# Optimization experiments

Measured on AMD Instinct MI355X. Metric: run time of the kernel, lower is better.

The kernel has to match this reference:

```python
import jax, jax.numpy as jnp
import numpy as np

G = 16          # graphs per side
NPG = 512       # nodes per graph
NSIDE = G * NPG # 8192 nodes per side
N = 2 * NSIDE   # 16384 nodes in combined batched graph
EPG = 4096      # edges per graph
E = 2 * G * EPG # 131072 edges
IN = 64; HID = 64; NH = 8; NC = 3
ALPHA = 0.2; EPS = 1e-5


def setup_inputs() -> dict:
    key = jax.random.key(0)
    ks = jax.random.split(key, 20)
    s = 0.05
    off = jnp.repeat(jnp.arange(2 * G, dtype=jnp.int32) * NPG, EPG)
    return {
        'nbd1': jax.random.normal(ks[0], (NSIDE, IN), jnp.float32),
        'nbd2': jax.random.normal(ks[1], (NSIDE, IN), jnp.float32),
        'ebd': jax.random.normal(ks[2], (E, IN), jnp.float32),
        'src': jax.random.randint(ks[3], (E,), 0, NPG, jnp.int32) + off,
        'dst': jax.random.randint(ks[4], (E,), 0, NPG, jnp.int32) + off,
        'node_gid': jnp.repeat(jnp.arange(2 * G, dtype=jnp.int32), NPG),
        'projW': jax.random.normal(ks[5], (4 * IN, HID), jnp.float32) * s,
        'W1': jax.random.normal(ks[6], (IN, NH * HID), jnp.float32) * s,
        'al1': jax.random.normal(ks[7], (NH, HID), jnp.float32) * s,
        'ar1': jax.random.normal(ks[8], (NH, HID), jnp.float32) * s,
        'ae1': jax.random.normal(ks[9], (NH, HID), jnp.float32) * s,
        'W2': jax.random.normal(ks[10], (NH * HID, NH * HID), jnp.float32) * s,
        'al2': jax.random.normal(ks[11], (NH, HID), jnp.float32) * s,
        'ar2': jax.random.normal(ks[12], (NH, HID), jnp.float32) * s,
        'ae2': jax.random.normal(ks[13], (NH, HID), jnp.float32) * s,
        'bn1_g': jnp.ones((2 * NH * HID,), jnp.float32),
        'bn1_b': jnp.zeros((2 * NH * HID,), jnp.float32),
        'fc1_W': jax.random.normal(ks[14], (2 * NH * HID, HID), jnp.float32) * s,
        'fc1_b': jnp.zeros((HID,), jnp.float32),
        'bn2_g': jnp.ones((HID,), jnp.float32),
        'bn2_b': jnp.zeros((HID,), jnp.float32),
        'fc2_W': jax.random.normal(ks[15], (HID, NC), jnp.float32) * s,
        'fc2_b': jnp.zeros((NC,), jnp.float32),
    }


def _segment_softmax(s, seg, n):
    # s: [E, H]; softmax over edges sharing the same destination node
    m = jax.ops.segment_max(s, seg, num_segments=n)
    ex = jnp.exp(s - m[seg])
    z = jax.ops.segment_sum(ex, seg, num_segments=n)
    return ex / jnp.maximum(z[seg], 1e-9)


def _gat_layer(hn, he, src, dst, n, W, al, ar, ae):
    nh, d = al.shape
    ft = (hn @ W).reshape(n, nh, d)            # [N,H,D]
    eft = (he @ W).reshape(-1, nh, d)          # [E,H,D]
    a1 = jnp.einsum('nhd,hd->nh', ft, al)
    a2 = jnp.einsum('nhd,hd->nh', ft, ar)
    a3 = jnp.einsum('ehd,hd->eh', eft, ae)
    a = a1[src] + a3 + a2[dst]                 # [E,H]
    a = jnp.where(a > 0, a, ALPHA * a)         # LeakyReLU(0.2)
    alpha = _segment_softmax(a, dst, n)[:, :, None]  # [E,H,1]
    f_cat = eft * alpha + ft[src] * alpha      # weighted edge + weighted src feat
    nft = jax.ops.segment_sum(f_cat, dst, num_segments=n)
    ret1 = jax.nn.elu(nft.reshape(n, nh * d))
    ret2 = jax.nn.elu(f_cat.reshape(f_cat.shape[0], nh * d))
    return ret1, ret2


def _bn(x, g, b):
    mu = jnp.mean(x, axis=0)
    v = jnp.var(x, axis=0)
    return (x - mu) * jax.lax.rsqrt(v + EPS) * g + b


def _forward(nbd1, nbd2, ebd, src, dst, node_gid, projW,
             W1, al1, ar1, ae1, W2, al2, ar2, ae2,
             bn1_g, bn1_b, fc1_W, fc1_b, bn2_g, bn2_b, fc2_W, fc2_b):
    # Node alignment (cross-graph soft attention, 2-D tensors as in source)
    att = nbd1 @ nbd2.T                                   # [N1,N2]
    x1a = jax.nn.softmax(att, axis=-1) @ nbd2
    x2a = jax.nn.softmax(att.T, axis=-1) @ nbd1
    q1 = jnp.concatenate([nbd1, x1a, nbd1 - x1a, nbd1 * x1a], axis=-1)
    q2 = jnp.concatenate([nbd2, x2a, nbd2 - x2a, nbd2 * x2a], axis=-1)
    h1 = jax.nn.relu(q1 @ projW)
    h2 = jax.nn.relu(q2 @ projW)
    h_n = jnp.concatenate([h1, h2], axis=0)               # [N,HID]
    h_e = ebd
    h_n, h_e = _gat_layer(h_n, h_e, src, dst, N, W1, al1, ar1, ae1)
    h_n, h_e = _gat_layer(h_n, h_e, src, dst, N, W2, al2, ar2, ae2)
    # dgl.mean_nodes
    cnt = jax.ops.segment_sum(jnp.ones((N,), h_n.dtype), node_gid, num_segments=2 * G)
    hg = jax.ops.segment_sum(h_n, node_gid, num_segments=2 * G) / cnt[:, None]
    x = jnp.concatenate([hg[:G], hg[G:2 * G]], axis=1)    # [G, 2*NH*HID]
    x = _bn(x, bn1_g, bn1_b)
    x = jax.nn.relu(x @ fc1_W + fc1_b)
    x = _bn(x, bn2_g, bn2_b)
    return x @ fc2_W + fc2_b                              # [G, NC]


def reference(nbd1, nbd2, ebd, src, dst, node_gid, projW,
              W1, al1, ar1, ae1, W2, al2, ar2, ae2,
              bn1_g, bn1_b, fc1_W, fc1_b, bn2_g, bn2_b, fc2_W, fc2_b):
    return _forward(nbd1, nbd2, ebd, src, dst, node_gid, projW,
                    W1, al1, ar1, ae1, W2, al2, ar2, ae2,
                    bn1_g, bn1_b, fc1_W, fc1_b, bn2_g, bn2_b, fc2_W, fc2_b)
```

## Files before the change

### kernel.cpp

```cpp
#include <hip/hip_runtime.h>


#define NSd 8192
#define NNd 16384
#define NEd 131072
#define KSPLIT 8

typedef unsigned short u16;
typedef unsigned int   u32;
typedef short bf16x8 __attribute__((ext_vector_type(8)));
typedef float f32x4  __attribute__((ext_vector_type(4)));
typedef float f32x16 __attribute__((ext_vector_type(16)));

__device__ __forceinline__ float bf2f(u16 u){ return __uint_as_float(((u32)u) << 16); }
__device__ __forceinline__ u16 f2bf(float f){
  u32 u = __float_as_uint(f);
  u += 0x7fffu + ((u >> 16) & 1u);
  return (u16)(u >> 16);
}
__device__ __forceinline__ u32 pkbf(float a, float b){
  u32 r;
  asm("v_cvt_pk_bf16_f32 %0, %1, %2" : "=v"(r) : "v"(a), "v"(b));
  return r;
}
__device__ __forceinline__ void pl32swap(u32& a, u32& b){
  auto r = __builtin_amdgcn_permlane32_swap(a, b, false, false);
  a = r[0]; b = r[1];
}
__device__ __forceinline__ float eluf(float x){ return x > 0.f ? x : expm1f(x); }
__device__ __forceinline__ float leaky(float x){ return x > 0.f ? x : 0.2f * x; }
__device__ __forceinline__ float ldin(const void* p, size_t i, int fl){
  return fl ? bf2f(((const u16*)p)[i]) : ((const float*)p)[i];
}
__device__ __forceinline__ void lse_merge(float& m, float& z, float om, float oz){
  float M = fmaxf(m, om);
  z = z * __expf(m - M) + oz * __expf(om - M);
  m = M;
}

static constexpr size_t OFF_WF   = 0;
static constexpr size_t OFF_CB   = 1529600;
static constexpr size_t OFF_U    = 1584896;
static constexpr size_t OFF_W1B  = 18362112;
static constexpr size_t OFF_W2B  = 18427648;
static constexpr size_t OFF_WE2B = 18951936;
static constexpr size_t OFF_WE1B = 18968320;
static constexpr size_t OFF_AL1  = 35139328;
static constexpr size_t OFF_SA   = 39333632;
static constexpr size_t OFF_HNA  = 43527936;
static constexpr size_t OFF_AN2  = 60305152;
static constexpr size_t OFF_DEG  = 77082368;
static constexpr size_t OFF_RP   = 77147904;
static constexpr size_t OFF_FILL = 77213696;
static constexpr size_t OFF_CIDX = 77279232;
static constexpr size_t OFF_RBIG = 77803520;
static constexpr size_t OFF_T    = 111357952;
static constexpr size_t OFF_XCAT = 144912384;
static constexpr size_t OFF_FLAG = 144977920;
static constexpr size_t WS_NEED  = 144978176;

static constexpr size_t T_X1A = 0;
static constexpr size_t T_X2A = 2097152;
static constexpr size_t T_HN0 = 4194304;
static constexpr size_t T_PZ  = 4194304;
static constexpr size_t T_AN1 = 8388608;
static constexpr size_t T_S   = 9437184;
static constexpr size_t T_Y   = 0;
static constexpr size_t T_Y1G = 0;
static constexpr size_t R_G2  = 16777216;

static constexpr int WO_PROJ = 0,      WO_W1 = 16384;
static constexpr int WO_AL1 = 49152,   WO_AR1 = 49664,  WO_AE1 = 50176;
static constexpr int WO_W2  = 50688;
static constexpr int WO_AL2 = 312832,  WO_AR2 = 313344, WO_AE2 = 313856;
static constexpr int WO_B1G = 314368,  WO_B1B = 315392;
static constexpr int WO_F1W = 316416,  WO_F1B = 381952;
static constexpr int WO_B2G = 382016,  WO_B2B = 382080;
static constexpr int WO_F2W = 382144,  WO_F2B = 382336;
static constexpr int WO_END = 382339;

static constexpr int CB_WC1 = 0;
static constexpr int CB_WE1 = 1024;
static constexpr int CB_WC2 = 1536;
static constexpr int CB_WE2 = 9728;
static constexpr int CB_END = 13824;

__global__ __launch_bounds__(256) void detect_k(const u16* __restrict__ p, int* __restrict__ flag){
  __shared__ int bad;
  if (threadIdx.x == 0) bad = 0;
  __syncthreads();
  int b = 0;
  for (int i = threadIdx.x; i < 1024; i += 256){
    float f = bf2f(p[i]);
    if (!(fabsf(f) <= 100.f)) b++;
  }
  atomicAdd(&bad, b);
  __syncthreads();
  if (threadIdx.x == 0) *flag = (bad == 0) ? 1 : 0;
}

struct P17 { const void* p[17]; };

__global__ __launch_bounds__(256) void convw_k(P17 ps, float* __restrict__ wf, const int* __restrict__ flagp){
  const int i = blockIdx.x * 256 + threadIdx.x;
  if (i >= WO_END) return;
  const int fl = *flagp;
  const int ends[17] = {16384,49152,49664,50176,50688,312832,313344,313856,314368,
                        315392,316416,381952,382016,382080,382144,382336,382339};
  int seg = 0;
  while (i >= ends[seg]) seg++;
  const int start = seg ? ends[seg-1] : 0;
  wf[i] = ldin(ps.p[seg], i - start, fl);
}

__global__ __launch_bounds__(256) void wprep_k(const float* __restrict__ wf, u16* __restrict__ w1t,
                                               u16* __restrict__ w2t, float* __restrict__ cb,
                                               u16* __restrict__ we2b, u16* __restrict__ we1b){
  const int i = blockIdx.x * 256 + threadIdx.x;
  if (i < 32768){
    const int c = i >> 6, k = i & 63;
    w1t[i] = f2bf(wf[WO_W1 + k * 512 + c]);
    return;
  }
  if (i < 294912){
    const int j = i - 32768;
    const int c = j >> 9, k = j & 511;
    w2t[j] = f2bf(wf[WO_W2 + k * 512 + c]);
    return;
  }
  const int j = i - 294912;
  if (j >= CB_END + 4096 + 512) return;
  if (j >= CB_END + 4096){ we1b[512 + (j - CB_END - 4096)] = 0; return; }
  if (j >= CB_END){ we2b[4096 + (j - CB_END)] = 0; return; }
  float acc = 0.f;
  if (j < 1024){
    const int o = j >> 6, d = j & 63, h = o & 7;
    const float* a = wf + ((o >> 3) ? WO_AR1 : WO_AL1) + h * 64;
    for (int dp = 0; dp < 64; dp++) acc += wf[WO_W1 + d * 512 + h * 64 + dp] * a[dp];
    cb[CB_WC1 + j] = acc;
  } else if (j < 1536){
    const int jj = j - 1024, h = jj >> 6, d = jj & 63;
    for (int dp = 0; dp < 64; dp++) acc += wf[WO_W1 + d * 512 + h * 64 + dp] * wf[WO_AE1 + h * 64 + dp];
    cb[CB_WE1 + jj] = acc;
    we1b[jj] = f2bf(acc);
  } else if (j < 9728){
    const int jj = j - 1536, o = jj >> 9, c = jj & 511, h = o & 7;
    for (int dp = 0; dp < 64; dp++){
      const float av = (o >> 3) ? wf[WO_AR2 + h * 64 + dp]
                                : (wf[WO_AL2 + h * 64 + dp] - wf[WO_AE2 + h * 64 + dp]);
      acc += wf[WO_W2 + c * 512 + h * 64 + dp] * av;
    }
    cb[CB_WC2 + jj] = acc;
  } else {
    const int jj = j - 9728, h = jj >> 9, c = jj & 511;
    for (int dp = 0; dp < 64; dp++) acc += wf[WO_W2 + c * 512 + h * 64 + dp] * wf[WO_AE2 + h * 64 + dp];
    cb[CB_WE2 + jj] = acc;
    we2b[jj] = f2bf(acc);
  }
}

__global__ __launch_bounds__(256) void flash_mfma_k(const void* __restrict__ Qp, const void* __restrict__ Kp,
                                                    const int* __restrict__ flagp, float* __restrict__ pacc,
                                                    float* __restrict__ pz){
  const int fl = *flagp;
  __shared__ __align__(16) u16 Ks[2][32][64];
  __shared__ __align__(16) u16 Kt[2][64][40];
  const int t = threadIdx.x;
  const int w = t >> 6, l = t & 63;
  const int hi = l >> 5, ql = l & 31;
  const int q0 = blockIdx.x * 128;
  const int kbeg = blockIdx.y * 1024;
  const int sr = t & 31, scg = t >> 5;
  const int kp = t & 15, dq = t >> 4;

  bf16x8 bq[4];
  {
    const int qrow = q0 + w * 32 + ql;
    if (fl){
      const u16* qp = (const u16*)Qp + (size_t)qrow * 64 + hi * 8;
      #pragma unroll
      for (int s = 0; s < 4; s++) bq[s] = *(const bf16x8*)(qp + s * 16);
    } else {
      const float* qp = (const float*)Qp + (size_t)qrow * 64 + hi * 8;
      #pragma unroll
      for (int s = 0; s < 4; s++){
        union { u32 w_[4]; bf16x8 v; } u;
        #pragma unroll
        for (int i = 0; i < 4; i++) u.w_[i] = pkbf(qp[s*16 + 2*i], qp[s*16 + 2*i + 1]);
        bq[s] = u.v;
      }
    }
  }

  f32x16 accO0, accO1;
  #pragma unroll
  for (int i = 0; i < 16; i++){ accO0[i] = 0.f; accO1[i] = 0.f; }
  float lsum = 0.f;

  {
    const int kr = kbeg;
    if (fl){
      const u16* kb = (const u16*)Kp + (size_t)kr * 64;
      const uint4 s0 = *(const uint4*)(kb + (size_t)sr * 64 + scg * 8);
      const uint2 a0 = *(const uint2*)(kb + (size_t)(2*kp) * 64 + dq * 4);
      const uint2 b0 = *(const uint2*)(kb + (size_t)(2*kp + 1) * 64 + dq * 4);
      *(uint4*)((char*)&Ks[0][sr][0] + ((scg * 16) ^ ((sr & 7) << 4))) = s0;
      const u16* pa = (const u16*)&a0; const u16* pb = (const u16*)&b0;
      #pragma unroll
      for (int i = 0; i < 4; i++)
        *(u32*)&Kt[0][4*dq + i][2*kp] = (u32)pa[i] | ((u32)pb[i] << 16);
    } else {
      const float* kf = (const float*)Kp + (size_t)kr * 64;
      const float4 f0 = *(const float4*)(kf + (size_t)sr * 64 + scg * 8);
      const float4 f1 = *(const float4*)(kf + (size_t)sr * 64 + scg * 8 + 4);
      const float4 fa = *(const float4*)(kf + (size_t)(2*kp) * 64 + dq * 4);
      const float4 fb = *(const float4*)(kf + (size_t)(2*kp + 1) * 64 + dq * 4);
      union { u32 w_[4]; uint4 q; } uu;
      uu.w_[0] = pkbf(f0.x, f0.y); uu.w_[1] = pkbf(f0.z, f0.w);
      uu.w_[2] = pkbf(f1.x, f1.y); uu.w_[3] = pkbf(f1.z, f1.w);
      *(uint4*)((char*)&Ks[0][sr][0] + ((scg * 16) ^ ((sr & 7) << 4))) = uu.q;
      const float* faf = &fa.x; const float* fbf = &fb.x;
      #pragma unroll
      for (int i = 0; i < 4; i++)
        *(u32*)&Kt[0][4*dq + i][2*kp] = pkbf(faf[i], fbf[i]);
    }
  }

  for (int it = 0; it < 32; it++){
    const int cur = it & 1;
    __syncthreads();

    uint4 nKs; uint2 nKa, nKb;
    float4 nKsf0, nKsf1, nKaf, nKbf;
    const bool nx = (it + 1 < 32);
    if (nx){
      const int kr = kbeg + (it + 1) * 32;
      if (fl){
        const u16* kb = (const u16*)Kp + (size_t)kr * 64;
        nKs = *(const uint4*)(kb + (size_t)sr * 64 + scg * 8);
        nKa = *(const uint2*)(kb + (size_t)(2*kp) * 64 + dq * 4);
        nKb = *(const uint2*)(kb + (size_t)(2*kp + 1) * 64 + dq * 4);
      } else {
        const float* kf = (const float*)Kp + (size_t)kr * 64;
        nKsf0 = *(const float4*)(kf + (size_t)sr * 64 + scg * 8);
        nKsf1 = *(const float4*)(kf + (size_t)sr * 64 + scg * 8 + 4);
        nKaf  = *(const float4*)(kf + (size_t)(2*kp) * 64 + dq * 4);
        nKbf  = *(const float4*)(kf + (size_t)(2*kp + 1) * 64 + dq * 4);
      }
    }

    f32x16 accS;
    #pragma unroll
    for (int i = 0; i < 16; i++) accS[i] = 0.f;
    #pragma unroll
    for (int s = 0; s < 4; s++){
      const int byo = (s * 32 + hi * 16) ^ ((ql & 7) << 4);
      const bf16x8 a = *(const bf16x8*)((const char*)&Ks[cur][ql][0] + byo);
      accS = __builtin_amdgcn_mfma_f32_32x32x16_bf16(a, bq[s], accS, 0, 0, 0);
    }
    float p[16];
    #pragma unroll
    for (int r = 0; r < 16; r++) p[r] = exp2f(fmaf(accS[r], 1.44269504f, -46.1662413f));
    {
      const float s0 = (p[0] + p[1]) + (p[2] + p[3]);
      const float s1 = (p[4] + p[5]) + (p[6] + p[7]);
      const float s2 = (p[8] + p[9]) + (p[10] + p[11]);
      const float s3 = (p[12] + p[13]) + (p[14] + p[15]);
      lsum += (s0 + s1) + (s2 + s3);
    }
    u32 pk_[8];
    #pragma unroll
    for (int j = 0; j < 4; j++){
      pk_[2*j]     = pkbf(p[4*j],     p[4*j + 1]);
      pk_[2*j + 1] = pkbf(p[4*j + 2], p[4*j + 3]);
    }
    pl32swap(pk_[0], pk_[2]); pl32swap(pk_[1], pk_[3]);
    pl32swap(pk_[4], pk_[6]); pl32swap(pk_[5], pk_[7]);
    union { u32 w_[4]; bf16x8 v; } ua, ub;
    ua.w_[0] = pk_[0]; ua.w_[1] = pk_[1]; ua.w_[2] = pk_[2]; ua.w_[3] = pk_[3];
    ub.w_[0] = pk_[4]; ub.w_[1] = pk_[5]; ub.w_[2] = pk_[6]; ub.w_[3] = pk_[7];
    {
      const u16* kt0 = &Kt[cur][ql][hi * 8];
      accO0 = __builtin_amdgcn_mfma_f32_32x32x16_bf16(ua.v, *(const bf16x8*)kt0, accO0, 0, 0, 0);
      accO0 = __builtin_amdgcn_mfma_f32_32x32x16_bf16(ub.v, *(const bf16x8*)(kt0 + 16), accO0, 0, 0, 0);
      const u16* kt1 = &Kt[cur][32 + ql][hi * 8];
      accO1 = __builtin_amdgcn_mfma_f32_32x32x16_bf16(ua.v, *(const bf16x8*)kt1, accO1, 0, 0, 0);
      accO1 = __builtin_amdgcn_mfma_f32_32x32x16_bf16(ub.v, *(const bf16x8*)(kt1 + 16), accO1, 0, 0, 0);
    }

    if (nx){
      char* kd = (char*)&Ks[cur ^ 1][sr][0];
      const int byo = (scg * 16) ^ ((sr & 7) << 4);
      if (fl){
        *(uint4*)(kd + byo) = nKs;
        const u16* pa = (const u16*)&nKa; const u16* pb = (const u16*)&nKb;
        #pragma unroll
        for (int i = 0; i < 4; i++)
          *(u32*)&Kt[cur ^ 1][4*dq + i][2*kp] = (u32)pa[i] | ((u32)pb[i] << 16);
      } else {
        union { u32 w_[4]; uint4 q; } uu;
        uu.w_[0] = pkbf(nKsf0.x, nKsf0.y); uu.w_[1] = pkbf(nKsf0.z, nKsf0.w);
        uu.w_[2] = pkbf(nKsf1.x, nKsf1.y); uu.w_[3] = pkbf(nKsf1.z, nKsf1.w);
        *(uint4*)(kd + byo) = uu.q;
        const float* faf = &nKaf.x; const float* fbf = &nKbf.x;
        #pragma unroll
        for (int i = 0; i < 4; i++)
          *(u32*)&Kt[cur ^ 1][4*dq + i][2*kp] = pkbf(faf[i], fbf[i]);
      }
    }
  }

  const float zq = lsum + __shfl_xor(lsum, 32);
  const int rowb = q0 + w * 32;
  #pragma unroll
  for (int r = 0; r < 16; r++){
    const int m = (r & 3) + 8 * (r >> 2) + 4 * hi;
    float* pr = pacc + ((size_t)blockIdx.y * NSd + rowb + m) * 64;
    pr[ql]      = accO0[r];
    pr[32 + ql] = accO1[r];
  }
  if (hi == 0) pz[blockIdx.y * NSd + rowb + ql] = zq;
}

__global__ __launch_bounds__(256) void flash_merge_k(const float* __restrict__ pacc,
                                                     const float* __restrict__ pz, float* __restrict__ outp){
  const int t = threadIdx.x;
  const int r = blockIdx.x * 4 + (t >> 6);
  const int d = t & 63;
  float Zt = 0.f, v = 0.f;
  #pragma unroll
  for (int s = 0; s < KSPLIT; s++){
    Zt += pz[s * NSd + r];
    v  += pacc[((size_t)s * NSd + r) * 64 + d];
  }
  outp[(size_t)r * 64 + d] = v / Zt;
}

__global__ __launch_bounds__(256) void proj_k(const void* __restrict__ nbd1, const void* __restrict__ nbd2,
                                              const float* __restrict__ x1a, const float* __restrict__ x2a,
                                              const float* __restrict__ wf, float* __restrict__ hn0,
                                              const int* __restrict__ flagp){
  const int fl = *flagp;
  __shared__ float At[64][65], Bt[64][65];
  const int t = threadIdx.x, tx = t & 15, ty = t >> 4;
  const int m0 = blockIdx.x * 64;
  float acc[4][4] = {{0.f}};
  for (int kt = 0; kt < 256; kt += 64){
    __syncthreads();
    {
      const int i = t >> 2, c0 = (t & 3) * 16;
      const int mrow = m0 + i;
      const int side = mrow < NSd;
      const int mr = side ? mrow : mrow - NSd;
      const void* nb = side ? nbd1 : nbd2;
      const float* xa = side ? x1a : x2a;
      const int seg = kt >> 6;
      for (int c = 0; c < 16; c++){
        const int kk = c0 + c;
        const float nv = ldin(nb, (size_t)mr * 64 + kk, fl);
        const float av = xa[(size_t)mr * 64 + kk];
        At[i][kk] = (seg == 0) ? nv : (seg == 1) ? av : (seg == 2) ? (nv - av) : (nv * av);
      }
      const int kk = t >> 2;
      for (int c = 0; c < 16; c++) Bt[kk][c0 + c] = wf[WO_PROJ + (kt + kk) * 64 + c0 + c];
    }
    __syncthreads();
    #pragma unroll
    for (int k = 0; k < 64; k++){
      float a0 = At[ty*4+0][k], a1 = At[ty*4+1][k], a2 = At[ty*4+2][k], a3 = At[ty*4+3][k];
      float b0 = Bt[k][tx*4+0], b1 = Bt[k][tx*4+1], b2 = Bt[k][tx*4+2], b3 = Bt[k][tx*4+3];
      acc[0][0] = fmaf(a0,b0,acc[0][0]); acc[0][1] = fmaf(a0,b1,acc[0][1]); acc[0][2] = fmaf(a0,b2,acc[0][2]); acc[0][3] = fmaf(a0,b3,acc[0][3]);
      acc[1][0] = fmaf(a1,b0,acc[1][0]); acc[1][1] = fmaf(a1,b1,acc[1][1]); acc[1][2] = fmaf(a1,b2,acc[1][2]); acc[1][3] = fmaf(a1,b3,acc[1][3]);
      acc[2][0] = fmaf(a2,b0,acc[2][0]); acc[2][1] = fmaf(a2,b1,acc[2][1]); acc[2][2] = fmaf(a2,b2,acc[2][2]); acc[2][3] = fmaf(a2,b3,acc[2][3]);
      acc[3][0] = fmaf(a3,b0,acc[3][0]); acc[3][1] = fmaf(a3,b1,acc[3][1]); acc[3][2] = fmaf(a3,b2,acc[3][2]); acc[3][3] = fmaf(a3,b3,acc[3][3]);
    }
  }
  #pragma unroll
  for (int i = 0; i < 4; i++)
    #pragma unroll
    for (int j = 0; j < 4; j++)
      hn0[(size_t)(m0 + ty*4 + i) * 64 + tx*4 + j] = fmaxf(acc[i][j], 0.f);
}

__global__ __launch_bounds__(256) void an64_k(const float* __restrict__ hn0, const float* __restrict__ wc,
                                              float* __restrict__ an){
  const int id = blockIdx.x * 256 + threadIdx.x;
  const int n = id >> 4, o = id & 15;
  const float* row = hn0 + (size_t)n * 64;
  const float* wp = wc + o * 64;
  float acc = 0.f;
  for (int k = 0; k < 64; k += 4){
    const float4 r4 = *(const float4*)(row + k);
    const float4 w4 = *(const float4*)(wp + k);
    acc += r4.x*w4.x + r4.y*w4.y + r4.z*w4.z + r4.w*w4.w;
  }
  an[id] = acc;
}

__global__ __launch_bounds__(256) void anw_k(const u16* __restrict__ HNA, const float* __restrict__ wc,
                                             float* __restrict__ an){
  __shared__ float W[16][516];
  const int t = threadIdx.x;
  for (int i = t; i < 8192; i += 256) W[i >> 9][i & 511] = wc[i];
  __syncthreads();
  const int node = blockIdx.x * 64 + (t >> 2);
  const int cb0 = (t & 3) * 4;
  const u16* row = HNA + (size_t)node * 512;
  float acc[4] = {0.f, 0.f, 0.f, 0.f};
  for (int k = 0; k < 512; k += 4){
    const uint2 u = *(const uint2*)(row + k);
    const float r0 = bf2f((u16)(u.x & 0xffffu)), r1 = bf2f((u16)(u.x >> 16));
    const float r2 = bf2f((u16)(u.y & 0xffffu)), r3 = bf2f((u16)(u.y >> 16));
    #pragma unroll
    for (int j = 0; j < 4; j++){
      const float* wr = &W[cb0 + j][k];
      acc[j] += r0 * wr[0] + r1 * wr[1] + r2 * wr[2] + r3 * wr[3];
    }
  }
  #pragma unroll
  for (int j = 0; j < 4; j++) an[node * 16 + cb0 + j] = acc[j];
}

__global__ __launch_bounds__(256) void us1_k(const void* __restrict__ ebd, const float* __restrict__ hn0,
                                             const int* __restrict__ src, u16* __restrict__ Ub,
                                             const int* __restrict__ flagp){
  const int fl = *flagp;
  const int id = blockIdx.x * 256 + threadIdx.x;
  const int e = id >> 4, q = id & 15, d0 = q * 4;
  const int sn = src[e];
  float ev[4];
  if (fl){
    const uint2 u = *(const uint2*)((const u16*)ebd + (size_t)e * 64 + d0);
    ev[0] = bf2f((u16)(u.x & 0xffffu)); ev[1] = bf2f((u16)(u.x >> 16));
    ev[2] = bf2f((u16)(u.y & 0xffffu)); ev[3] = bf2f((u16)(u.y >> 16));
  } else {
    const float4 f = *(const float4*)((const float*)ebd + (size_t)e * 64 + d0);
    ev[0] = f.x; ev[1] = f.y; ev[2] = f.z; ev[3] = f.w;
  }
  const float4 hv = *(const float4*)(hn0 + (size_t)sn * 64 + d0);
  ushort4 o;
  o.x = f2bf(ev[0] + hv.x); o.y = f2bf(ev[1] + hv.y);
  o.z = f2bf(ev[2] + hv.z); o.w = f2bf(ev[3] + hv.w);
  *(ushort4*)(Ub + (size_t)e * 64 + d0) = o;
}

__global__ __launch_bounds__(256) void score1_k(const void* __restrict__ ebd, const u16* __restrict__ we1b,
                                                const float* __restrict__ an, const int* __restrict__ src,
                                                const int* __restrict__ dst, const int* __restrict__ cidx,
                                                float* __restrict__ S, const int* __restrict__ flagp){
  __shared__ int Se[64], De[64], Ee[64];
  const int t = threadIdx.x;
  const int w = t >> 6, lane = t & 63;
  const int col = lane & 15, quad = lane >> 4;
  const int p0 = blockIdx.x * 64;
  if (t < 64){ const int e = cidx[p0 + t]; Ee[t] = e; Se[t] = src[e]; De[t] = dst[e]; }
  __syncthreads();
  const int fl = *flagp;
  const int ea = Ee[w*16 + col];
  bf16x8 a0, a1;
  if (fl){
    const u16* ap = (const u16*)ebd + (size_t)ea * 64;
    a0 = *(const bf16x8*)(ap + quad*8);
    a1 = *(const bf16x8*)(ap + 32 + quad*8);
  } else {
    const float* ap = (const float*)ebd + (size_t)ea * 64;
    union { u32 w_[4]; bf16x8 v; } u0, u1;
    #pragma unroll
    for (int i = 0; i < 4; i++){
      u0.w_[i] = pkbf(ap[quad*8 + 2*i],      ap[quad*8 + 2*i + 1]);
      u1.w_[i] = pkbf(ap[32 + quad*8 + 2*i], ap[32 + quad*8 + 2*i + 1]);
    }
    a0 = u0.v; a1 = u1.v;
  }
  const u16* brow = we1b + (size_t)col * 64;
  const bf16x8 b0 = *(const bf16x8*)(brow + quad*8);
  const bf16x8 b1 = *(const bf16x8*)(brow + 32 + quad*8);
  f32x4 acc = (f32x4){0.f, 0.f, 0.f, 0.f};
  acc = __builtin_amdgcn_mfma_f32_16x16x32_bf16(a0, b0, acc, 0, 0, 0);
  acc = __builtin_amdgcn_mfma_f32_16x16x32_bf16(a1, b1, acc, 0, 0, 0);
  if (col < 8){
    #pragma unroll
    for (int i = 0; i < 4; i++){
      const int rl = w*16 + quad*4 + i;
      S[(size_t)(p0 + rl) * 8 + col] = leaky(an[Se[rl]*16 + col] + acc[i] + an[De[rl]*16 + 8 + col]);
    }
  }
}

__global__ __launch_bounds__(256) void segalpha_pos_k(const float* __restrict__ S, const int* __restrict__ rp,
                                                      float* __restrict__ AL){
  const int node = blockIdx.x * 4 + (threadIdx.x >> 6);
  const int l = threadIdx.x & 63;
  const int h = l & 7, i0 = l >> 3;
  const int beg = rp[node], end = rp[node + 1];
  float m = -1e30f, z = 0.f;
  for (int base = beg; base < end; base += 8){
    const int idx = base + i0;
    float v = -1e30f, cc = 0.f;
    if (idx < end){ v = S[(size_t)idx * 8 + h]; cc = 1.f; }
    lse_merge(m, z, v, cc);
  }
  #pragma unroll
  for (int off = 8; off < 64; off <<= 1){
    float om = __shfl_xor(m, off), oz = __shfl_xor(z, off);
    lse_merge(m, z, om, oz);
  }
  const float rz = 1.f / fmaxf(z, 1e-9f);
  for (int base = beg; base < end; base += 8){
    const int idx = base + i0;
    if (idx < end)
      AL[(size_t)idx * 8 + h] = __expf(S[(size_t)idx * 8 + h] - m) * rz;
  }
}

__global__ __launch_bounds__(256) void g1b_k(const float* __restrict__ AL, const u16* __restrict__ Ub,
                                             const int* __restrict__ rp, const int* __restrict__ cidx,
                                             u16* __restrict__ G1b){
  const int n = blockIdx.x;
  const int t = threadIdx.x;
  const int d = t & 63, hh = t >> 6;
  const int beg = rp[n], end = rp[n + 1];
  float a0 = 0.f, a1 = 0.f;
  for (int idx = beg; idx < end; idx++){
    const int e = cidx[idx];
    const float uv = bf2f(Ub[(size_t)e * 64 + d]);
    a0 = fmaf(AL[(size_t)idx * 8 + hh],     uv, a0);
    a1 = fmaf(AL[(size_t)idx * 8 + hh + 4], uv, a1);
  }
  G1b[(size_t)(n * 8 + hh)     * 64 + d] = f2bf(a0);
  G1b[(size_t)(n * 8 + hh + 4) * 64 + d] = f2bf(a1);
}

__global__ __launch_bounds__(256) void nft1m_k(const u16* __restrict__ G1b, const u16* __restrict__ W1T,
                                               u16* __restrict__ HNA){
  const int t = threadIdx.x;
  const int w = t >> 6, lane = t & 63;
  const int col = lane & 15, quad = lane >> 4;
  const int h = blockIdx.y;
  const int nl0 = blockIdx.x * 32;
  const int mt = (w & 1) * 16;
  const int nb = (w >> 1) * 2;
  const u16* arow = G1b + ((size_t)(nl0 + mt + col) * 8 + h) * 64;
  const bf16x8 a0 = *(const bf16x8*)(arow + quad*8);
  const bf16x8 a1 = *(const bf16x8*)(arow + 32 + quad*8);
  #pragma unroll
  for (int nn = 0; nn < 2; nn++){
    const int nt = nb + nn;
    const u16* brow = W1T + (size_t)(h*64 + nt*16 + col) * 64;
    const bf16x8 b0 = *(const bf16x8*)(brow + quad*8);
    const bf16x8 b1 = *(const bf16x8*)(brow + 32 + quad*8);
    f32x4 acc = (f32x4){0.f, 0.f, 0.f, 0.f};
    acc = __builtin_amdgcn_mfma_f32_16x16x32_bf16(a0, b0, acc, 0, 0, 0);
    acc = __builtin_amdgcn_mfma_f32_16x16x32_bf16(a1, b1, acc, 0, 0, 0);
    #pragma unroll
    for (int i = 0; i < 4; i++)
      HNA[(size_t)(nl0 + mt + quad*4 + i) * 512 + h*64 + nt*16 + col] = f2bf(eluf(acc[i]));
  }
}

__global__ __launch_bounds__(256) void y3_k(const u16* __restrict__ Ub, const float* __restrict__ AL1,
                                            const u16* __restrict__ HNA, const u16* __restrict__ W1T,
                                            const int* __restrict__ src, const int* __restrict__ cidx,
                                            u16* __restrict__ Y, const int s2){
  __shared__ __align__(16) u16 Us[32][72];
  __shared__ float als[256];
  __shared__ int Es[32], Ss[32];
  const int t = threadIdx.x;
  const int w = t >> 6, lane = t & 63;
  const int col = lane & 15, quad = lane >> 4;
  const int mw = (w & 1) * 16;
  const int hw = (w >> 1) * 4;
  const int ep0 = s2 * 32768 + blockIdx.x * 32;
  if (t < 32){ const int e = cidx[ep0 + t]; Es[t] = e; Ss[t] = src[e]; }
  als[t] = AL1[(size_t)ep0 * 8 + t];
  __syncthreads();
  {
    const int r = t >> 3, seg = (t & 7) * 8;
    *(ushort4*)&Us[r][seg]     = *(const ushort4*)(Ub + (size_t)Es[r] * 64 + seg);
    *(ushort4*)&Us[r][seg + 4] = *(const ushort4*)(Ub + (size_t)Es[r] * 64 + seg + 4);
  }
  __syncthreads();
  const bf16x8 a0 = *(const bf16x8*)&Us[mw + col][quad*8];
  const bf16x8 a1 = *(const bf16x8*)&Us[mw + col][32 + quad*8];
  #pragma unroll
  for (int hh = 0; hh < 4; hh++){
    const int h = hw + hh;
    #pragma unroll
    for (int nt = 0; nt < 4; nt++){
      const u16* brow = W1T + (size_t)(h*64 + nt*16 + col) * 64;
      const bf16x8 b0 = *(const bf16x8*)(brow + quad*8);
      const bf16x8 b1 = *(const bf16x8*)(brow + 32 + quad*8);
      f32x4 acc = (f32x4){0.f, 0.f, 0.f, 0.f};
      acc = __builtin_amdgcn_mfma_f32_16x16x32_bf16(a0, b0, acc, 0, 0, 0);
      acc = __builtin_amdgcn_mfma_f32_16x16x32_bf16(a1, b1, acc, 0, 0, 0);
      #pragma unroll
      for (int i = 0; i < 4; i++){
        const int er = mw + quad*4 + i;
        const float v = eluf(als[er*8 + h] * acc[i])
                      + bf2f(HNA[(size_t)Ss[er] * 512 + h*64 + nt*16 + col]);
        Y[(size_t)(blockIdx.x*32 + er) * 512 + h*64 + nt*16 + col] = f2bf(v);
      }
    }
  }
}

__global__ __launch_bounds__(256) void score2_k(const u16* __restrict__ Y, const u16* __restrict__ we2b,
                                                const float* __restrict__ AN2, const int* __restrict__ src,
                                                const int* __restrict__ dst, const int* __restrict__ cidx,
                                                float* __restrict__ SA, const int s2){
  __shared__ int Se[64], De[64];
  const int t = threadIdx.x;
  const int w = t >> 6, lane = t & 63;
  const int col = lane & 15, quad = lane >> 4;
  const int p0 = blockIdx.x * 64;
  const int gbase = s2 * 32768;
  if (t < 64){ const int e = cidx[gbase + p0 + t]; Se[t] = src[e]; De[t] = dst[e]; }
  __syncthreads();
  const u16* arow = Y + (size_t)(p0 + w*16 + col) * 512;
  const u16* brow = we2b + (size_t)col * 512;
  f32x4 acc = (f32x4){0.f, 0.f, 0.f, 0.f};
  #pragma unroll
  for (int ks = 0; ks < 16; ks++){
    const bf16x8 a = *(const bf16x8*)(arow + ks*32 + quad*8);
    const bf16x8 b = *(const bf16x8*)(brow + ks*32 + quad*8);
    acc = __builtin_amdgcn_mfma_f32_16x16x32_bf16(a, b, acc, 0, 0, 0);
  }
  if (col < 8){
    #pragma unroll
    for (int i = 0; i < 4; i++){
      const int rl = w*16 + quad*4 + i;
      const size_t pos = gbase + p0 + rl;
      SA[pos * 8 + col] = leaky(AN2[Se[rl]*16 + col] + acc[i] + AN2[De[rl]*16 + 8 + col]);
    }
  }
}

__global__ __launch_bounds__(256) void sg2_k(const u16* __restrict__ Y, const int* __restrict__ rp,
                                             const float* __restrict__ SA, u16* __restrict__ G2,
                                             const int s){
  __shared__ float sc[64][8];
  __shared__ float mh[8], rzh[8];
  const int t = threadIdx.x;
  const int nl = blockIdx.x;
  const int n = s * 2048 + nl;
  const int beg = rp[n], end = rp[n + 1], m = end - beg;
  const int base = (s >> 1) * 32768;
  const bool small = (m <= 64);
  {
    const int h = t >> 5, l32 = t & 31;
    float mm = -1e30f, zz = 0.f;
    for (int i = l32; i < m; i += 32)
      lse_merge(mm, zz, SA[(size_t)(beg + i) * 8 + h], 1.f);
    #pragma unroll
    for (int off = 1; off < 32; off <<= 1){
      const float om = __shfl_xor(mm, off), oz = __shfl_xor(zz, off);
      lse_merge(mm, zz, om, oz);
    }
    if (l32 == 0){ mh[h] = mm; rzh[h] = 1.f / fmaxf(zz, 1e-9f); }
  }
  __syncthreads();
  if (small){
    for (int idx = t; idx < m * 8; idx += 256){
      const int i = idx >> 3, h = idx & 7;
      sc[i][h] = __expf(SA[(size_t)(beg + i) * 8 + h] - mh[h]) * rzh[h];
    }
  }
  __syncthreads();
  {
    const int d0 = t * 2;
    float ac[8][2] = {{0.f}};
    for (int i = 0; i < m; i++){
      const int epl = beg + i - base;
      const u32 yv = *(const u32*)(Y + (size_t)epl * 512 + d0);
      const float y0 = bf2f((u16)(yv & 0xffffu)), y1 = bf2f((u16)(yv >> 16));
      float al[8];
      if (small){
        #pragma unroll
        for (int h = 0; h < 8; h++) al[h] = sc[i][h];
      } else {
        #pragma unroll
        for (int h = 0; h < 8; h++)
          al[h] = __expf(SA[(size_t)(beg + i) * 8 + h] - mh[h]) * rzh[h];
      }
      #pragma unroll
      for (int h = 0; h < 8; h++){
        ac[h][0] = fmaf(al[h], y0, ac[h][0]);
        ac[h][1] = fmaf(al[h], y1, ac[h][1]);
      }
    }
    #pragma unroll
    for (int h = 0; h < 8; h++){
      const u32 o = (u32)f2bf(ac[h][0]) | ((u32)f2bf(ac[h][1]) << 16);
      *(u32*)(G2 + ((size_t)nl * 8 + h) * 512 + d0) = o;
    }
  }
}

__global__ __launch_bounds__(256) void nft2m_k(const u16* __restrict__ G2, const u16* __restrict__ W2T,
                                               u16* __restrict__ HNB, const int s){
  const int t = threadIdx.x;
  const int w = t >> 6, lane = t & 63;
  const int col = lane & 15, quad = lane >> 4;
  const int h = blockIdx.y;
  const int nl0 = blockIdx.x * 32;
  const int mt = (w & 1) * 16;
  const int nb = (w >> 1) * 2;
  const u16* arow = G2 + ((size_t)((nl0 + mt + col) * 8) + h) * 512;
  #pragma unroll
  for (int nn = 0; nn < 2; nn++){
    const int nt = nb + nn;
    const u16* brow = W2T + (size_t)(h*64 + nt*16 + col) * 512;
    f32x4 acc = (f32x4){0.f, 0.f, 0.f, 0.f};
    #pragma unroll
    for (int ks = 0; ks < 16; ks++){
      const bf16x8 a = *(const bf16x8*)(arow + ks*32 + quad*8);
      const bf16x8 b = *(const bf16x8*)(brow + ks*32 + quad*8);
      acc = __builtin_amdgcn_mfma_f32_16x16x32_bf16(a, b, acc, 0, 0, 0);
    }
    #pragma unroll
    for (int i = 0; i < 4; i++)
      HNB[(size_t)(s*2048 + nl0 + mt + quad*4 + i) * 512 + h*64 + nt*16 + col] = f2bf(eluf(acc[i]));
  }
}

__global__ __launch_bounds__(256) void hist_k(const int* __restrict__ dst, int* __restrict__ deg){
  const int e = blockIdx.x * 256 + threadIdx.x;
  if (e < NEd) atomicAdd(&deg[dst[e]], 1);
}
__global__ __launch_bounds__(256) void scan_k(const int* __restrict__ deg, int* __restrict__ rp,
                                              int* __restrict__ fill){
  __shared__ int wsum[4];
  const int t = threadIdx.x;
  const int lane = t & 63, wid = t >> 6;
  const int base = t * 64;
  int s = 0;
  for (int i = 0; i < 64; i++) s += deg[base + i];
  int v = s;
  #pragma unroll
  for (int off = 1; off < 64; off <<= 1){
    const int u = __shfl_up(v, off);
    if (lane >= off) v += u;
  }
  if (lane == 63) wsum[wid] = v;
  __syncthreads();
  int add = 0;
  #pragma unroll
  for (int wq = 0; wq < 4; wq++) if (wq < wid) add += wsum[wq];
  int off0 = add + v - s;
  for (int i = 0; i < 64; i++){
    rp[base + i] = off0; fill[base + i] = off0;
    off0 += deg[base + i];
  }
  if (t == 255) rp[NNd] = off0;
}
__global__ __launch_bounds__(256) void scatter_k(const int* __restrict__ dst, int* __restrict__ fill,
                                                 int* __restrict__ cidx){
  const int e = blockIdx.x * 256 + threadIdx.x;
  if (e < NEd){
    int pos = atomicAdd(&fill[dst[e]], 1);
    cidx[pos] = e;
  }
}

__global__ __launch_bounds__(256) void mean_k(const u16* __restrict__ HNB, float* __restrict__ xcat){
  const int sg = blockIdx.x >> 3, chunk = blockIdx.x & 7;
  const int t = threadIdx.x;
  const int g = (sg < 16) ? sg : sg - 16;
  const int half = (sg < 16) ? 0 : 1;
  const int c0 = t * 2;
  float s0 = 0.f, s1 = 0.f;
  const u16* base = HNB + ((size_t)sg * 512 + chunk * 64) * 512;
  for (int n = 0; n < 64; n++){
    const u32 u = *(const u32*)(base + (size_t)n * 512 + c0);
    s0 += bf2f((u16)(u & 0xffffu));
    s1 += bf2f((u16)(u >> 16));
  }
  atomicAdd(&xcat[g * 1024 + half * 512 + c0],     s0 * (1.f / 512.f));
  atomicAdd(&xcat[g * 1024 + half * 512 + c0 + 1], s1 * (1.f / 512.f));
}

__global__ __launch_bounds__(256) void fc1_k(const float* __restrict__ xcat, const float* __restrict__ wf,
                                             float* __restrict__ y1g){
  __shared__ float xs[1024];
  __shared__ float ps[4][64];
  const int t = threadIdx.x, g = blockIdx.x;
  for (int j = t; j < 1024; j += 256){
    float mu = 0.f;
    #pragma unroll
    for (int gg = 0; gg < 16; gg++) mu += xcat[gg * 1024 + j];
    mu *= (1.f / 16.f);
    float var = 0.f;
    #pragma unroll
    for (int gg = 0; gg < 16; gg++){ const float d = xcat[gg * 1024 + j] - mu; var += d * d; }
    var *= (1.f / 16.f);
    const float sc = rsqrtf(var + 1e-5f) * wf[WO_B1G + j];
    xs[j] = (xcat[g * 1024 + j] - mu) * sc + wf[WO_B1B + j];
  }
  __syncthreads();
  const int c = t & 63, kq = t >> 6;
  float acc = 0.f;
  #pragma unroll 4
  for (int k = kq * 256; k < kq * 256 + 256; k++)
    acc = fmaf(xs[k], wf[WO_F1W + k * 64 + c], acc);
  ps[kq][c] = acc;
  __syncthreads();
  if (t < 64){
    const float a = ps[0][t] + ps[1][t] + ps[2][t] + ps[3][t] + wf[WO_F1B + t];
    y1g[g * 64 + t] = fmaxf(a, 0.f);
  }
}

__global__ __launch_bounds__(256) void head2_k(const float* __restrict__ y1g, const float* __restrict__ wf,
                                               void* __restrict__ outp, const int* __restrict__ flagp){
  __shared__ float y1s[16][64];
  __shared__ float mu2s[64], sc2s[64];
  const int t = threadIdx.x;
  for (int i = t; i < 1024; i += 256) y1s[i >> 6][i & 63] = y1g[i];
  __syncthreads();
  if (t < 64){
    float mu = 0.f;
    #pragma unroll
    for (int g = 0; g < 16; g++) mu += y1s[g][t];
    mu *= (1.f / 16.f);
    float var = 0.f;
    #pragma unroll
    for (int g = 0; g < 16; g++){ const float d = y1s[g][t] - mu; var += d * d; }
    var *= (1.f / 16.f);
    mu2s[t] = mu; sc2s[t] = rsqrtf(var + 1e-5f) * wf[WO_B2G + t];
  }
  __syncthreads();
  if (t < 48){
    const int gg = t / 3, c = t % 3;
    float acc = wf[WO_F2B + c];
    #pragma unroll
    for (int k = 0; k < 64; k++){
      const float y2 = (y1s[gg][k] - mu2s[k]) * sc2s[k] + wf[WO_B2B + k];
      acc = fmaf(y2, wf[WO_F2W + k * 3 + c], acc);
    }
    if (*flagp) ((u16*)outp)[t] = f2bf(acc);
    else        ((float*)outp)[t] = acc;
  }
}

extern "C" void kernel_launch(void* const* d_in, const int* in_sizes, int n_in,
                              void* d_out, int out_size, void* d_ws, size_t ws_size,
                              hipStream_t stream) {
  (void)in_sizes; (void)n_in; (void)out_size;
  if (ws_size < WS_NEED) return;

  const int* src = (const int*)d_in[3];
  const int* dst = (const int*)d_in[4];
  char* w = (char*)d_ws;

  float* wf   = (float*)(w + OFF_WF);
  float* cb   = (float*)(w + OFF_CB);
  u16*   Ub   = (u16*)(w + OFF_U);
  u16*   W1T  = (u16*)(w + OFF_W1B);
  u16*   W2T  = (u16*)(w + OFF_W2B);
  u16*   we2b = (u16*)(w + OFF_WE2B);
  u16*   we1b = (u16*)(w + OFF_WE1B);
  float* AL1  = (float*)(w + OFF_AL1);
  float* SA   = (float*)(w + OFF_SA);
  u16*   HNA  = (u16*)(w + OFF_HNA);
  float* AN2  = (float*)(w + OFF_AN2);
  int*   deg  = (int*)(w + OFF_DEG);
  int*   rp   = (int*)(w + OFF_RP);
  int*   fill = (int*)(w + OFF_FILL);
  int*   cidx = (int*)(w + OFF_CIDX);
  float* rbig = (float*)(w + OFF_RBIG);
  float* xcat = (float*)(w + OFF_XCAT);
  int*   flag = (int*)(w + OFF_FLAG);

  float* x1a  = (float*)(w + OFF_T + T_X1A);
  float* x2a  = (float*)(w + OFF_T + T_X2A);
  float* hn0  = (float*)(w + OFF_T + T_HN0);
  float* AN1  = (float*)(w + OFF_T + T_AN1);
  float* S    = (float*)(w + OFF_T + T_S);
  u16*   Y    = (u16*)(w + OFF_T + T_Y);
  float* y1g  = (float*)(w + OFF_T + T_Y1G);

  float* pacc = rbig;
  float* pz   = (float*)(w + OFF_T + T_PZ);
  u16*   G1b  = (u16*)(w + OFF_RBIG);
  u16*   HNB  = (u16*)(w + OFF_RBIG);
  u16*   G2   = (u16*)(w + OFF_RBIG + R_G2);

  detect_k<<<1, 256, 0, stream>>>((const u16*)d_in[0], flag);
  P17 ps;
  for (int i = 0; i < 17; i++) ps.p[i] = d_in[6 + i];
  convw_k<<<(WO_END + 255) / 256, 256, 0, stream>>>(ps, wf, flag);
  wprep_k<<<(294912 + CB_END + 4096 + 512 + 255) / 256, 256, 0, stream>>>(wf, W1T, W2T, cb, we2b, we1b);

  hipMemsetAsync(deg, 0, NNd * sizeof(int), stream);
  hist_k<<<NEd / 256, 256, 0, stream>>>(dst, deg);
  scan_k<<<1, 256, 0, stream>>>(deg, rp, fill);
  scatter_k<<<NEd / 256, 256, 0, stream>>>(dst, fill, cidx);

  flash_mfma_k<<<dim3(64, KSPLIT), 256, 0, stream>>>(d_in[0], d_in[1], flag, pacc, pz);
  flash_merge_k<<<NSd / 4, 256, 0, stream>>>(pacc, pz, x1a);
  flash_mfma_k<<<dim3(64, KSPLIT), 256, 0, stream>>>(d_in[1], d_in[0], flag, pacc, pz);
  flash_merge_k<<<NSd / 4, 256, 0, stream>>>(pacc, pz, x2a);

  proj_k<<<NNd / 64, 256, 0, stream>>>(d_in[0], d_in[1], x1a, x2a, wf, hn0, flag);

  an64_k<<<NNd * 16 / 256, 256, 0, stream>>>(hn0, cb + CB_WC1, AN1);
  us1_k<<<NEd * 16 / 256, 256, 0, stream>>>(d_in[2], hn0, src, Ub, flag);
  score1_k<<<NEd / 64, 256, 0, stream>>>(d_in[2], we1b, AN1, src, dst, cidx, S, flag);
  segalpha_pos_k<<<NNd / 4, 256, 0, stream>>>(S, rp, AL1);
  g1b_k<<<NNd, 256, 0, stream>>>(AL1, Ub, rp, cidx, G1b);
  nft1m_k<<<dim3(NNd / 32, 8), 256, 0, stream>>>(G1b, W1T, HNA);

  anw_k<<<NNd / 64, 256, 0, stream>>>(HNA, cb + CB_WC2, AN2);

  for (int s2 = 0; s2 < 4; s2++){
    y3_k<<<1024, 256, 0, stream>>>(Ub, AL1, HNA, W1T, src, cidx, Y, s2);
    score2_k<<<512, 256, 0, stream>>>(Y, we2b, AN2, src, dst, cidx, SA, s2);
    for (int sub = 0; sub < 2; sub++){
      const int s = s2 * 2 + sub;
      sg2_k<<<2048, 256, 0, stream>>>(Y, rp, SA, G2, s);
      nft2m_k<<<dim3(64, 8), 256, 0, stream>>>(G2, W2T, HNB, s);
    }
  }

  hipMemsetAsync(xcat, 0, 16 * 1024 * sizeof(float), stream);
  mean_k<<<256, 256, 0, stream>>>(HNB, xcat);
  fc1_k<<<16, 256, 0, stream>>>(xcat, wf, y1g);
  head2_k<<<1, 256, 0, stream>>>(y1g, wf, d_out, flag);
}
```

Before: 810.5 us.

## Fuse edge prep, softmax+aggregate, and layer-2 scoring into segment kernels

Merges us1_k and an64_k into one launch split by block index. Merges segalpha_pos_k and g1b_k into one per-node kernel that keeps attention weights in shared memory. Also folds score2_k into the per-destination aggregation kernel: one wave computes the MFMA scores for that node's edges into shared memory before the softmax and aggregation. This cuts launches and S/SA round trips through global memory, but the score MFMA now runs on a single wave per block while the other waves wait at a barrier.

```diff
diff --git a/kernel.cpp b/kernel.cpp
--- a/kernel.cpp
+++ b/kernel.cpp
@@ -382,19 +382,43 @@
       hn0[(size_t)(m0 + ty*4 + i) * 64 + tx*4 + j] = fmaxf(acc[i][j], 0.f);
 }
 
-__global__ __launch_bounds__(256) void an64_k(const float* __restrict__ hn0, const float* __restrict__ wc,
-                                              float* __restrict__ an){
-  const int id = blockIdx.x * 256 + threadIdx.x;
-  const int n = id >> 4, o = id & 15;
-  const float* row = hn0 + (size_t)n * 64;
-  const float* wp = wc + o * 64;
-  float acc = 0.f;
-  for (int k = 0; k < 64; k += 4){
-    const float4 r4 = *(const float4*)(row + k);
-    const float4 w4 = *(const float4*)(wp + k);
-    acc += r4.x*w4.x + r4.y*w4.y + r4.z*w4.z + r4.w*w4.w;
-  }
-  an[id] = acc;
+__global__ __launch_bounds__(256) void usan_k(const void* __restrict__ ebd, const float* __restrict__ hn0,
+                                              const int* __restrict__ src, u16* __restrict__ Ub,
+                                              const float* __restrict__ wc, float* __restrict__ an,
+                                              const int* __restrict__ flagp){
+  const int b = blockIdx.x, t = threadIdx.x;
+  if (b < 8192){
+    const int fl = *flagp;
+    const int id = b * 256 + t;
+    const int e = id >> 4, q = id & 15, d0 = q * 4;
+    const int sn = src[e];
+    float ev[4];
+    if (fl){
+      const uint2 u = *(const uint2*)((const u16*)ebd + (size_t)e * 64 + d0);
+      ev[0] = bf2f((u16)(u.x & 0xffffu)); ev[1] = bf2f((u16)(u.x >> 16));
+      ev[2] = bf2f((u16)(u.y & 0xffffu)); ev[3] = bf2f((u16)(u.y >> 16));
+    } else {
+      const float4 f = *(const float4*)((const float*)ebd + (size_t)e * 64 + d0);
+      ev[0] = f.x; ev[1] = f.y; ev[2] = f.z; ev[3] = f.w;
+    }
+    const float4 hv = *(const float4*)(hn0 + (size_t)sn * 64 + d0);
+    ushort4 o;
+    o.x = f2bf(ev[0] + hv.x); o.y = f2bf(ev[1] + hv.y);
+    o.z = f2bf(ev[2] + hv.z); o.w = f2bf(ev[3] + hv.w);
+    *(ushort4*)(Ub + (size_t)e * 64 + d0) = o;
+  } else {
+    const int id = (b - 8192) * 256 + t;
+    const int n = id >> 4, o = id & 15;
+    const float* row = hn0 + (size_t)n * 64;
+    const float* wp = wc + o * 64;
+    float acc = 0.f;
+    for (int k = 0; k < 64; k += 4){
+      const float4 r4 = *(const float4*)(row + k);
+      const float4 w4 = *(const float4*)(wp + k);
+      acc += r4.x*w4.x + r4.y*w4.y + r4.z*w4.z + r4.w*w4.w;
+    }
+    an[id] = acc;
+  }
 }
 
 __global__ __launch_bounds__(256) void anw_k(const u16* __restrict__ HNA, const float* __restrict__ wc,
@@ -419,29 +443,6 @@
   }
   #pragma unroll
   for (int j = 0; j < 4; j++) an[node * 16 + cb0 + j] = acc[j];
-}
-
-__global__ __launch_bounds__(256) void us1_k(const void* __restrict__ ebd, const float* __restrict__ hn0,
-                                             const int* __restrict__ src, u16* __restrict__ Ub,
-                                             const int* __restrict__ flagp){
-  const int fl = *flagp;
-  const int id = blockIdx.x * 256 + threadIdx.x;
-  const int e = id >> 4, q = id & 15, d0 = q * 4;
-  const int sn = src[e];
-  float ev[4];
-  if (fl){
-    const uint2 u = *(const uint2*)((const u16*)ebd + (size_t)e * 64 + d0);
-    ev[0] = bf2f((u16)(u.x & 0xffffu)); ev[1] = bf2f((u16)(u.x >> 16));
-    ev[2] = bf2f((u16)(u.y & 0xffffu)); ev[3] = bf2f((u16)(u.y >> 16));
-  } else {
-    const float4 f = *(const float4*)((const float*)ebd + (size_t)e * 64 + d0);
-    ev[0] = f.x; ev[1] = f.y; ev[2] = f.z; ev[3] = f.w;
-  }
-  const float4 hv = *(const float4*)(hn0 + (size_t)sn * 64 + d0);
-  ushort4 o;
-  o.x = f2bf(ev[0] + hv.x); o.y = f2bf(ev[1] + hv.y);
-  o.z = f2bf(ev[2] + hv.z); o.w = f2bf(ev[3] + hv.w);
-  *(ushort4*)(Ub + (size_t)e * 64 + d0) = o;
 }
 
 __global__ __launch_bounds__(256) void score1_k(const void* __restrict__ ebd, const u16* __restrict__ we1b,
@@ -487,45 +488,44 @@
   }
 }
 
-__global__ __launch_bounds__(256) void segalpha_pos_k(const float* __restrict__ S, const int* __restrict__ rp,
-                                                      float* __restrict__ AL){
-  const int node = blockIdx.x * 4 + (threadIdx.x >> 6);
-  const int l = threadIdx.x & 63;
-  const int h = l & 7, i0 = l >> 3;
-  const int beg = rp[node], end = rp[node + 1];
-  float m = -1e30f, z = 0.f;
-  for (int base = beg; base < end; base += 8){
-    const int idx = base + i0;
-    float v = -1e30f, cc = 0.f;
-    if (idx < end){ v = S[(size_t)idx * 8 + h]; cc = 1.f; }
-    lse_merge(m, z, v, cc);
-  }
-  #pragma unroll
-  for (int off = 8; off < 64; off <<= 1){
-    float om = __shfl_xor(m, off), oz = __shfl_xor(z, off);
-    lse_merge(m, z, om, oz);
-  }
-  const float rz = 1.f / fmaxf(z, 1e-9f);
-  for (int base = beg; base < end; base += 8){
-    const int idx = base + i0;
-    if (idx < end)
-      AL[(size_t)idx * 8 + h] = __expf(S[(size_t)idx * 8 + h] - m) * rz;
-  }
-}
-
-__global__ __launch_bounds__(256) void g1b_k(const float* __restrict__ AL, const u16* __restrict__ Ub,
-                                             const int* __restrict__ rp, const int* __restrict__ cidx,
-                                             u16* __restrict__ G1b){
-  const int n = blockIdx.x;
-  const int t = threadIdx.x;
+__global__ __launch_bounds__(256) void sga_g1_k(const float* __restrict__ S, const int* __restrict__ rp,
+                                                const int* __restrict__ cidx, const u16* __restrict__ Ub,
+                                                float* __restrict__ AL, u16* __restrict__ G1b){
+  __shared__ float sc[64][8];
+  __shared__ float mh[8], rzh[8];
+  const int n = blockIdx.x, t = threadIdx.x;
+  const int beg = rp[n], end = rp[n + 1], m = end - beg;
+  const bool small = (m <= 64);
+  {
+    const int h = t >> 5, l32 = t & 31;
+    float mm = -1e30f, zz = 0.f;
+    for (int i = l32; i < m; i += 32)
+      lse_merge(mm, zz, S[(size_t)(beg + i) * 8 + h], 1.f);
+    #pragma unroll
+    for (int off = 1; off < 32; off <<= 1){
+      const float om = __shfl_xor(mm, off), oz = __shfl_xor(zz, off);
+      lse_merge(mm, zz, om, oz);
+    }
+    if (l32 == 0){ mh[h] = mm; rzh[h] = 1.f / fmaxf(zz, 1e-9f); }
+  }
+  __syncthreads();
+  for (int idx = t; idx < m * 8; idx += 256){
+    const int i = idx >> 3, h = idx & 7;
+    const float al = __expf(S[(size_t)(beg + i) * 8 + h] - mh[h]) * rzh[h];
+    AL[(size_t)(beg + i) * 8 + h] = al;
+    if (small) sc[i][h] = al;
+  }
+  __syncthreads();
   const int d = t & 63, hh = t >> 6;
-  const int beg = rp[n], end = rp[n + 1];
   float a0 = 0.f, a1 = 0.f;
-  for (int idx = beg; idx < end; idx++){
-    const int e = cidx[idx];
+  for (int i = 0; i < m; i++){
+    const int e = cidx[beg + i];
     const float uv = bf2f(Ub[(size_t)e * 64 + d]);
-    a0 = fmaf(AL[(size_t)idx * 8 + hh],     uv, a0);
-    a1 = fmaf(AL[(size_t)idx * 8 + hh + 4], uv, a1);
+    float al0, al1;
+    if (small){ al0 = sc[i][hh]; al1 = sc[i][hh + 4]; }
+    else { al0 = AL[(size_t)(beg + i) * 8 + hh]; al1 = AL[(size_t)(beg + i) * 8 + hh + 4]; }
+    a0 = fmaf(al0, uv, a0);
+    a1 = fmaf(al1, uv, a1);
   }
   G1b[(size_t)(n * 8 + hh)     * 64 + d] = f2bf(a0);
   G1b[(size_t)(n * 8 + hh + 4) * 64 + d] = f2bf(a1);
@@ -604,53 +604,59 @@
   }
 }
 
-__global__ __launch_bounds__(256) void score2_k(const u16* __restrict__ Y, const u16* __restrict__ we2b,
-                                                const float* __restrict__ AN2, const int* __restrict__ src,
-                                                const int* __restrict__ dst, const int* __restrict__ cidx,
-                                                float* __restrict__ SA, const int s2){
-  __shared__ int Se[64], De[64];
+__global__ __launch_bounds__(256) void sgf_k(const u16* __restrict__ Y, const u16* __restrict__ we2b,
+                                             const float* __restrict__ AN2, const int* __restrict__ src,
+                                             const int* __restrict__ cidx, const int* __restrict__ rp,
+                                             float* __restrict__ SA, u16* __restrict__ G2, const int s){
+  __shared__ float sc[64][8];
+  __shared__ float mh[8], rzh[8];
+  __shared__ int Se[64];
   const int t = threadIdx.x;
   const int w = t >> 6, lane = t & 63;
   const int col = lane & 15, quad = lane >> 4;
-  const int p0 = blockIdx.x * 64;
-  const int gbase = s2 * 32768;
-  if (t < 64){ const int e = cidx[gbase + p0 + t]; Se[t] = src[e]; De[t] = dst[e]; }
-  __syncthreads();
-  const u16* arow = Y + (size_t)(p0 + w*16 + col) * 512;
-  const u16* brow = we2b + (size_t)col * 512;
-  f32x4 acc = (f32x4){0.f, 0.f, 0.f, 0.f};
-  #pragma unroll
-  for (int ks = 0; ks < 16; ks++){
-    const bf16x8 a = *(const bf16x8*)(arow + ks*32 + quad*8);
-    const bf16x8 b = *(const bf16x8*)(brow + ks*32 + quad*8);
-    acc = __builtin_amdgcn_mfma_f32_16x16x32_bf16(a, b, acc, 0, 0, 0);
-  }
-  if (col < 8){
-    #pragma unroll
-    for (int i = 0; i < 4; i++){
-      const int rl = w*16 + quad*4 + i;
-      const size_t pos = gbase + p0 + rl;
-      SA[pos * 8 + col] = leaky(AN2[Se[rl]*16 + col] + acc[i] + AN2[De[rl]*16 + 8 + col]);
-    }
-  }
-}
-
-__global__ __launch_bounds__(256) void sg2_k(const u16* __restrict__ Y, const int* __restrict__ rp,
-                                             const float* __restrict__ SA, u16* __restrict__ G2,
-                                             const int s){
-  __shared__ float sc[64][8];
-  __shared__ float mh[8], rzh[8];
-  const int t = threadIdx.x;
   const int nl = blockIdx.x;
   const int n = s * 2048 + nl;
   const int beg = rp[n], end = rp[n + 1], m = end - beg;
   const int base = (s >> 1) * 32768;
+  const int lbeg = beg - base;
   const bool small = (m <= 64);
+  if (small && t < m) Se[t] = src[cidx[beg + t]];
+  __syncthreads();
+  if (w == 0){
+    for (int t0 = 0; t0 < m; t0 += 16){
+      int ar = lbeg + t0 + col; if (ar > 32767) ar = 32767;
+      const u16* arow = Y + (size_t)ar * 512;
+      const u16* brow = we2b + (size_t)col * 512;
+      f32x4 acc = (f32x4){0.f, 0.f, 0.f, 0.f};
+      #pragma unroll
+      for (int ks = 0; ks < 16; ks++){
+        const bf16x8 a = *(const bf16x8*)(arow + ks*32 + quad*8);
+        const bf16x8 b = *(const bf16x8*)(brow + ks*32 + quad*8);
+        acc = __builtin_amdgcn_mfma_f32_16x16x32_bf16(a, b, acc, 0, 0, 0);
+      }
+      if (col < 8){
+        const float anD = AN2[n * 16 + 8 + col];
+        #pragma unroll
+        for (int i = 0; i < 4; i++){
+          const int r = t0 + quad*4 + i;
+          if (r < m){
+            const int se = small ? Se[r] : src[cidx[beg + r]];
+            const float v = leaky(AN2[se * 16 + col] + acc[i] + anD);
+            if (small) sc[r][col] = v;
+            else       SA[(size_t)(beg + r) * 8 + col] = v;
+          }
+        }
+      }
+    }
+  }
+  __syncthreads();
   {
     const int h = t >> 5, l32 = t & 31;
     float mm = -1e30f, zz = 0.f;
-    for (int i = l32; i < m; i += 32)
-      lse_merge(mm, zz, SA[(size_t)(beg + i) * 8 + h], 1.f);
+    for (int i = l32; i < m; i += 32){
+      const float v = small ? sc[i][h] : SA[(size_t)(beg + i) * 8 + h];
+      lse_merge(mm, zz, v, 1.f);
+    }
     #pragma unroll
     for (int off = 1; off < 32; off <<= 1){
       const float om = __shfl_xor(mm, off), oz = __shfl_xor(zz, off);
@@ -662,7 +668,7 @@
   if (small){
     for (int idx = t; idx < m * 8; idx += 256){
       const int i = idx >> 3, h = idx & 7;
-      sc[i][h] = __expf(SA[(size_t)(beg + i) * 8 + h] - mh[h]) * rzh[h];
+      sc[i][h] = __expf(sc[i][h] - mh[h]) * rzh[h];
     }
   }
   __syncthreads();
@@ -670,8 +676,7 @@
     const int d0 = t * 2;
     float ac[8][2] = {{0.f}};
     for (int i = 0; i < m; i++){
-      const int epl = beg + i - base;
-      const u32 yv = *(const u32*)(Y + (size_t)epl * 512 + d0);
+      const u32 yv = *(const u32*)(Y + (size_t)(lbeg + i) * 512 + d0);
       const float y0 = bf2f((u16)(yv & 0xffffu)), y1 = bf2f((u16)(yv >> 16));
       float al[8];
       if (small){
@@ -903,21 +908,18 @@
 
   proj_k<<<NNd / 64, 256, 0, stream>>>(d_in[0], d_in[1], x1a, x2a, wf, hn0, flag);
 
-  an64_k<<<NNd * 16 / 256, 256, 0, stream>>>(hn0, cb + CB_WC1, AN1);
-  us1_k<<<NEd * 16 / 256, 256, 0, stream>>>(d_in[2], hn0, src, Ub, flag);
+  usan_k<<<8192 + 1024, 256, 0, stream>>>(d_in[2], hn0, src, Ub, cb + CB_WC1, AN1, flag);
   score1_k<<<NEd / 64, 256, 0, stream>>>(d_in[2], we1b, AN1, src, dst, cidx, S, flag);
-  segalpha_pos_k<<<NNd / 4, 256, 0, stream>>>(S, rp, AL1);
-  g1b_k<<<NNd, 256, 0, stream>>>(AL1, Ub, rp, cidx, G1b);
+  sga_g1_k<<<NNd, 256, 0, stream>>>(S, rp, cidx, Ub, AL1, G1b);
   nft1m_k<<<dim3(NNd / 32, 8), 256, 0, stream>>>(G1b, W1T, HNA);
 
   anw_k<<<NNd / 64, 256, 0, stream>>>(HNA, cb + CB_WC2, AN2);
 
   for (int s2 = 0; s2 < 4; s2++){
     y3_k<<<1024, 256, 0, stream>>>(Ub, AL1, HNA, W1T, src, cidx, Y, s2);
-    score2_k<<<512, 256, 0, stream>>>(Y, we2b, AN2, src, dst, cidx, SA, s2);
     for (int sub = 0; sub < 2; sub++){
       const int s = s2 * 2 + sub;
-      sg2_k<<<2048, 256, 0, stream>>>(Y, rp, SA, G2, s);
+      sgf_k<<<2048, 256, 0, stream>>>(Y, we2b, AN2, src, cidx, rp, SA, G2, s);
       nft2m_k<<<dim3(64, 8), 256, 0, stream>>>(G2, W2T, HNB, s);
     }
   }
```

New measurement: 863.9 us. +6.6%, slower.
